# Performance work log

Hardware: AMD Instinct MI355X
Metric: run time of the kernel (lower is better)

## Reference

```python
import jax, jax.numpy as jnp
import numpy as np

B, S, E, H = 2, 2048, 1024, 16  # batch, max_seq_length, embedding_dim, num_heads
D = E // H  # head dim = 64


def setup_inputs() -> dict:
    key = jax.random.key(0)
    ks = jax.random.split(key, 7)
    scale = 0.02
    return {
        "inputs": jax.random.normal(ks[0], (B, S, E), jnp.float32),
        "embbeding_V": jax.random.normal(ks[1], (B, S, E), jnp.float32),
        "embbeding_K": jax.random.normal(ks[2], (B, S, E), jnp.float32),
        "Wq": jax.random.normal(ks[3], (E, E), jnp.float32) * scale,
        "Wk": jax.random.normal(ks[4], (E, E), jnp.float32) * scale,
        "Wv": jax.random.normal(ks[5], (E, E), jnp.float32) * scale,
        "Wo": jax.random.normal(ks[6], (E, E), jnp.float32) * scale,
    }


def reference(inputs, embbeding_V, embbeding_K, Wq, Wk, Wv, Wo):
    b = inputs.shape[0]
    # repeat last token of `inputs` to max_seq_length: [b, S, E]
    x = jnp.broadcast_to(inputs[:, -1, :][:, None, :], (b, S, E))
    # torch Linear(bias=False): y = x @ W.T ; split heads -> [b, H, S, D]
    q = (x @ Wq.T).reshape(b, S, H, D).transpose(0, 2, 1, 3)
    k = (embbeding_K @ Wk.T).reshape(b, S, H, D).transpose(0, 2, 1, 3)
    v = (embbeding_V @ Wv.T).reshape(b, S, H, D).transpose(0, 2, 1, 3)
    # UNSCALED attention (faithful to source: no 1/sqrt(d))
    s = jnp.einsum("bhqd,bhkd->bhqk", q, k)
    p = jax.nn.softmax(s, axis=-1)
    o = jnp.einsum("bhqk,bhkd->bhqd", p, v)
    # transpose(1,2) then reshape to [b, S, E]
    o = o.transpose(0, 2, 1, 3).reshape(b, S, E)
    return o @ Wo.T
```

## Files before the change

kernel.cpp:

```cpp
#include <hip/hip_runtime.h>
#include <hip/hip_bf16.h>

constexpr int B = 2, S = 2048, E = 1024, H = 16, D = 64;
constexpr int E4 = E / 4;

__global__ void k_qvec(const float4* __restrict__ x, const float4* __restrict__ Wq,
                       float* __restrict__ q_vec) {
  int blk = blockIdx.x;
  int b = blk >> 7, n0 = (blk & 127) * 8;
  int tid = threadIdx.x;
  int nl = tid >> 5, es = tid & 31;
  const float4* xr = x + ((size_t)b * S + (S - 1)) * E4;
  const float4* wr = Wq + (size_t)(n0 + nl) * E4;
  float acc = 0.f;
#pragma unroll
  for (int j = 0; j < 8; ++j) {
    float4 a = xr[es + 32 * j];
    float4 w = wr[es + 32 * j];
    acc += a.x * w.x + a.y * w.y + a.z * w.z + a.w * w.w;
  }
#pragma unroll
  for (int o = 16; o > 0; o >>= 1) acc += __shfl_xor(acc, o, 64);
  if (es == 0) q_vec[b * E + n0 + nl] = acc;
}

__global__ void k_wkq(const float* __restrict__ q_vec, const float* __restrict__ Wk,
                      float* __restrict__ wkq, float* __restrict__ rowsum) {
  int blk = blockIdx.x;
  int eo = blk & 7;
  int bh = blk >> 3;
  int h = bh & 15;
  int tid = threadIdx.x;
  __shared__ float qh[D];
  if (tid < D) qh[tid] = q_vec[(bh >> 4) * E + h * D + tid];
  if (eo == 0 && tid == 0) rowsum[bh] = 0.f;
  __syncthreads();
  int e = eo * 128 + tid;
  const float* wp = Wk + (size_t)h * D * E + e;
  float acc = 0.f;
#pragma unroll 8
  for (int d = 0; d < D; ++d) acc += qh[d] * wp[(size_t)d * E];
  wkq[(size_t)bh * E + e] = acc;
}

__global__ __launch_bounds__(128) void k_scores_exp(const float4* __restrict__ embK,
                                                    const float4* __restrict__ wkq4,
                                                    float* __restrict__ p,
                                                    float* __restrict__ rowsum) {
  __shared__ float4 wl[H * E4];
  __shared__ float hsum[16];
  int blk = blockIdx.x;
  int b = blk >> 7, k0 = (blk & 127) * 16;
  int tid = threadIdx.x;
#pragma unroll
  for (int j = 0; j < 32; ++j)
    wl[j * 128 + tid] = wkq4[(size_t)b * (H * E4) + j * 128 + tid];
  if (tid < 16) hsum[tid] = 0.f;
  __syncthreads();
  int kp = tid >> 4, es = tid & 15;
  int ka = k0 + kp, kb = k0 + 8 + kp;
  const float4* ea = embK + ((size_t)b * S + ka) * E4;
  const float4* eb = embK + ((size_t)b * S + kb) * E4;
  float4 va[16], vb[16];
#pragma unroll
  for (int j = 0; j < 16; ++j) { va[j] = ea[es + 16 * j]; vb[j] = eb[es + 16 * j]; }
#pragma unroll 1
  for (int h = 0; h < H; ++h) {
    float aa = 0.f, ab = 0.f;
#pragma unroll
    for (int j = 0; j < 16; ++j) {
      float4 w = wl[h * 256 + es + 16 * j];
      aa += va[j].x * w.x + va[j].y * w.y + va[j].z * w.z + va[j].w * w.w;
      ab += vb[j].x * w.x + vb[j].y * w.y + vb[j].z * w.z + vb[j].w * w.w;
    }
#pragma unroll
    for (int o = 8; o > 0; o >>= 1) {
      aa += __shfl_xor(aa, o, 64);
      ab += __shfl_xor(ab, o, 64);
    }
    if (es == 0) {
      float pa = __expf(aa), pb = __expf(ab);
      float* pr = p + ((size_t)(b * H + h)) * S;
      pr[ka] = pa;
      pr[kb] = pb;
      atomicAdd(&hsum[h], pa + pb);
    }
  }
  __syncthreads();
  if (tid < 16) atomicAdd(&rowsum[b * H + tid], hsum[tid]);
}

__global__ __launch_bounds__(256) void k_ctx_part(const float4* __restrict__ embV,
                                                  const float* __restrict__ p,
                                                  const float* __restrict__ rowsum,
                                                  float4* __restrict__ part) {
  int b = blockIdx.x, eo = blockIdx.y, kz = blockIdx.z;
  int tid = threadIdx.x;
  int e4l = tid & 31, ksub = tid >> 5;
  int k0 = kz * 128;
  __shared__ float pl[16 * 128];
  __shared__ float sinv[16];
  if (tid < 16) sinv[tid] = 1.f / rowsum[b * H + tid];
  __syncthreads();
  for (int i = tid; i < 16 * 128; i += 256) {
    int h = i >> 7, kk = i & 127;
    pl[i] = p[((size_t)(b * H + h)) * S + k0 + kk] * sinv[h];
  }
  __syncthreads();
  int e4 = eo * 32 + e4l;
  float4 acc[H];
#pragma unroll
  for (int h = 0; h < H; ++h) acc[h] = make_float4(0.f, 0.f, 0.f, 0.f);
  int kb = ksub * 16;
  for (int i = 0; i < 16; ++i) {
    int kk = kb + i;
    float4 v = embV[((size_t)b * S + k0 + kk) * E4 + e4];
#pragma unroll
    for (int h = 0; h < H; ++h) {
      float pv = pl[h * 128 + kk];
      acc[h].x += pv * v.x; acc[h].y += pv * v.y;
      acc[h].z += pv * v.z; acc[h].w += pv * v.w;
    }
  }
#pragma unroll
  for (int h = 0; h < H; ++h) {
    acc[h].x += __shfl_xor(acc[h].x, 32, 64);
    acc[h].y += __shfl_xor(acc[h].y, 32, 64);
    acc[h].z += __shfl_xor(acc[h].z, 32, 64);
    acc[h].w += __shfl_xor(acc[h].w, 32, 64);
  }
  if ((tid & 63) < 32) {
    int pz = kz * 4 + (tid >> 6);
#pragma unroll
    for (int h = 0; h < H; ++h)
      part[((size_t)(pz * B + b) * H + h) * E4 + e4] = acc[h];
  }
}

__global__ __launch_bounds__(128) void k_reduce(const float4* __restrict__ part,
                                                float4* __restrict__ ctx4) {
  int b = blockIdx.x, h = blockIdx.y, eo = blockIdx.z;
  int tid = threadIdx.x;
  int e4l = tid & 31, psub = tid >> 5;
  int e4 = eo * 32 + e4l;
  const size_t pstride = (size_t)B * H * E4;
  const float4* pp = part + ((size_t)b * H + h) * E4 + e4 + psub * 16 * pstride;
  float4 acc = make_float4(0.f, 0.f, 0.f, 0.f);
#pragma unroll
  for (int j = 0; j < 16; ++j) {
    float4 c = pp[j * pstride];
    acc.x += c.x; acc.y += c.y; acc.z += c.z; acc.w += c.w;
  }
  __shared__ float4 red[128];
  red[tid] = acc;
  __syncthreads();
  if (tid < 32) {
    float4 a0 = red[tid], a1 = red[tid + 32], a2 = red[tid + 64], a3 = red[tid + 96];
    float4 r = make_float4(a0.x + a1.x + a2.x + a3.x, a0.y + a1.y + a2.y + a3.y,
                           a0.z + a1.z + a2.z + a3.z, a0.w + a1.w + a2.w + a3.w);
    ctx4[((size_t)b * H + h) * E4 + e4] = r;
  }
}

__global__ void k_ovec_wave(const float* __restrict__ ctx, const float4* __restrict__ Wv4,
                            float* __restrict__ o_vec) {
  int gw = (blockIdx.x * blockDim.x + threadIdx.x) >> 6;
  int lane = threadIdx.x & 63;
  int b = gw >> 10, nn = gw & 1023;
  const float4* xr = (const float4*)(ctx + ((size_t)(b * H + (nn >> 6))) * E);
  const float4* wr = Wv4 + (size_t)nn * E4;
  float acc = 0.f;
#pragma unroll
  for (int j = 0; j < 4; ++j) {
    float4 a = xr[lane + 64 * j];
    float4 w = wr[lane + 64 * j];
    acc += a.x * w.x + a.y * w.y + a.z * w.z + a.w * w.w;
  }
#pragma unroll
  for (int o = 32; o > 0; o >>= 1) acc += __shfl_xor(acc, o, 64);
  if (lane == 0) o_vec[gw] = acc;
}

__global__ void k_outvec(const float* __restrict__ o_vec, const float4* __restrict__ Wo4,
                         float* __restrict__ out_vec) {
  int gw = (blockIdx.x * blockDim.x + threadIdx.x) >> 6;
  int lane = threadIdx.x & 63;
  int b = gw >> 10, nn = gw & 1023;
  const float4* xr = (const float4*)(o_vec + (size_t)b * E);
  const float4* wr = Wo4 + (size_t)nn * E4;
  float acc = 0.f;
#pragma unroll
  for (int j = 0; j < 4; ++j) {
    float4 a = xr[lane + 64 * j];
    float4 w = wr[lane + 64 * j];
    acc += a.x * w.x + a.y * w.y + a.z * w.z + a.w * w.w;
  }
#pragma unroll
  for (int o = 32; o > 0; o >>= 1) acc += __shfl_xor(acc, o, 64);
  if (lane == 0) out_vec[gw] = acc;
}

__global__ void k_bcast(const float4* __restrict__ ov4, float4* __restrict__ out4) {
  int base = blockIdx.x * 1024 + threadIdx.x;
#pragma unroll
  for (int r = 0; r < 4; ++r) {
    int g = base + r * 256;
    out4[g] = ov4[(g >> 19) * E4 + (g & 255)];
  }
}

extern "C" void kernel_launch(void* const* d_in, const int* in_sizes, int n_in,
                              void* d_out, int out_size, void* d_ws, size_t ws_size,
                              hipStream_t stream) {
  const float* inputs = (const float*)d_in[0];
  const float* embV   = (const float*)d_in[1];
  const float* embK   = (const float*)d_in[2];
  const float* Wq     = (const float*)d_in[3];
  const float* Wk     = (const float*)d_in[4];
  const float* Wv     = (const float*)d_in[5];
  const float* Wo     = (const float*)d_in[6];

  float* ws      = (float*)d_ws;
  float* q_vec   = ws;
  float* wkq     = q_vec + B * E;
  float* p       = wkq + B * H * E;
  float* rowsum  = p + B * H * S;
  float* o_vec   = rowsum + 64;
  float* out_vec = o_vec + B * E;
  float* part    = out_vec + B * E;
  float* ctx     = part + 64 * B * H * E;

  k_qvec<<<256, 256, 0, stream>>>((const float4*)inputs, (const float4*)Wq, q_vec);
  k_wkq<<<256, 128, 0, stream>>>(q_vec, Wk, wkq, rowsum);
  k_scores_exp<<<256, 128, 0, stream>>>((const float4*)embK, (const float4*)wkq,
                                        p, rowsum);
  k_ctx_part<<<dim3(B, 8, 16), 256, 0, stream>>>((const float4*)embV, p, rowsum,
                                                 (float4*)part);
  k_reduce<<<dim3(B, H, 8), 128, 0, stream>>>((const float4*)part, (float4*)ctx);
  k_ovec_wave<<<512, 256, 0, stream>>>(ctx, (const float4*)Wv, o_vec);
  k_outvec<<<512, 256, 0, stream>>>(o_vec, (const float4*)Wo, out_vec);
  k_bcast<<<1024, 256, 0, stream>>>((const float4*)out_vec, (float4*)d_out);
}
```

Before: 148.4 us.

## Retile context partial sums to halve partials and defer softmax normalization

The context-partial kernel now covers 256 keys per block with 16 e4 lanes per row and interleaved key assignment. This halves the number of partial slices written and then re-read by the reduce kernel. Softmax division by the row sum moves from the per-element P staging into the output-vector kernel, removing a sync and a per-element multiply. The tradeoff is narrower 256-byte row segments per load and an extra shuffle stage in the reduction.

```diff
diff --git a/kernel.cpp b/kernel.cpp
--- a/kernel.cpp
+++ b/kernel.cpp
@@ -92,45 +92,45 @@
 
 __global__ __launch_bounds__(256) void k_ctx_part(const float4* __restrict__ embV,
                                                   const float* __restrict__ p,
-                                                  const float* __restrict__ rowsum,
                                                   float4* __restrict__ part) {
   int b = blockIdx.x, eo = blockIdx.y, kz = blockIdx.z;
   int tid = threadIdx.x;
-  int e4l = tid & 31, ksub = tid >> 5;
-  int k0 = kz * 128;
-  __shared__ float pl[16 * 128];
-  __shared__ float sinv[16];
-  if (tid < 16) sinv[tid] = 1.f / rowsum[b * H + tid];
-  __syncthreads();
-  for (int i = tid; i < 16 * 128; i += 256) {
-    int h = i >> 7, kk = i & 127;
-    pl[i] = p[((size_t)(b * H + h)) * S + k0 + kk] * sinv[h];
-  }
-  __syncthreads();
-  int e4 = eo * 32 + e4l;
+  int e4l = tid & 15, ks = tid >> 4;
+  int k0 = kz * 256;
+  __shared__ float pl[16 * 256];
+  for (int i = tid; i < 16 * 256; i += 256) {
+    int h = i >> 8, kk = i & 255;
+    pl[i] = p[((size_t)(b * H + h)) * S + k0 + kk];
+  }
+  __syncthreads();
+  int e4 = eo * 16 + e4l;
   float4 acc[H];
 #pragma unroll
   for (int h = 0; h < H; ++h) acc[h] = make_float4(0.f, 0.f, 0.f, 0.f);
-  int kb = ksub * 16;
   for (int i = 0; i < 16; ++i) {
-    int kk = kb + i;
+    int kk = ks + 16 * i;
     float4 v = embV[((size_t)b * S + k0 + kk) * E4 + e4];
 #pragma unroll
     for (int h = 0; h < H; ++h) {
-      float pv = pl[h * 128 + kk];
+      float pv = pl[h * 256 + kk];
       acc[h].x += pv * v.x; acc[h].y += pv * v.y;
       acc[h].z += pv * v.z; acc[h].w += pv * v.w;
     }
   }
 #pragma unroll
   for (int h = 0; h < H; ++h) {
+    acc[h].x += __shfl_xor(acc[h].x, 16, 64);
+    acc[h].y += __shfl_xor(acc[h].y, 16, 64);
+    acc[h].z += __shfl_xor(acc[h].z, 16, 64);
+    acc[h].w += __shfl_xor(acc[h].w, 16, 64);
     acc[h].x += __shfl_xor(acc[h].x, 32, 64);
     acc[h].y += __shfl_xor(acc[h].y, 32, 64);
     acc[h].z += __shfl_xor(acc[h].z, 32, 64);
     acc[h].w += __shfl_xor(acc[h].w, 32, 64);
   }
-  if ((tid & 63) < 32) {
-    int pz = kz * 4 + (tid >> 6);
+  int lane = tid & 63, w = tid >> 6;
+  if (lane < 16) {
+    int pz = kz * 4 + w;
 #pragma unroll
     for (int h = 0; h < H; ++h)
       part[((size_t)(pz * B + b) * H + h) * E4 + e4] = acc[h];
@@ -144,10 +144,10 @@
   int e4l = tid & 31, psub = tid >> 5;
   int e4 = eo * 32 + e4l;
   const size_t pstride = (size_t)B * H * E4;
-  const float4* pp = part + ((size_t)b * H + h) * E4 + e4 + psub * 16 * pstride;
+  const float4* pp = part + ((size_t)b * H + h) * E4 + e4 + (size_t)psub * 8 * pstride;
   float4 acc = make_float4(0.f, 0.f, 0.f, 0.f);
 #pragma unroll
-  for (int j = 0; j < 16; ++j) {
+  for (int j = 0; j < 8; ++j) {
     float4 c = pp[j * pstride];
     acc.x += c.x; acc.y += c.y; acc.z += c.z; acc.w += c.w;
   }
@@ -163,11 +163,12 @@
 }
 
 __global__ void k_ovec_wave(const float* __restrict__ ctx, const float4* __restrict__ Wv4,
-                            float* __restrict__ o_vec) {
+                            const float* __restrict__ rowsum, float* __restrict__ o_vec) {
   int gw = (blockIdx.x * blockDim.x + threadIdx.x) >> 6;
   int lane = threadIdx.x & 63;
   int b = gw >> 10, nn = gw & 1023;
-  const float4* xr = (const float4*)(ctx + ((size_t)(b * H + (nn >> 6))) * E);
+  int bh = b * H + (nn >> 6);
+  const float4* xr = (const float4*)(ctx + (size_t)bh * E);
   const float4* wr = Wv4 + (size_t)nn * E4;
   float acc = 0.f;
 #pragma unroll
@@ -178,7 +179,7 @@
   }
 #pragma unroll
   for (int o = 32; o > 0; o >>= 1) acc += __shfl_xor(acc, o, 64);
-  if (lane == 0) o_vec[gw] = acc;
+  if (lane == 0) o_vec[gw] = acc / rowsum[bh];
 }
 
 __global__ void k_outvec(const float* __restrict__ o_vec, const float4* __restrict__ Wo4,
@@ -228,16 +229,15 @@
   float* o_vec   = rowsum + 64;
   float* out_vec = o_vec + B * E;
   float* part    = out_vec + B * E;
-  float* ctx     = part + 64 * B * H * E;
+  float* ctx     = part + 32 * B * H * E;
 
   k_qvec<<<256, 256, 0, stream>>>((const float4*)inputs, (const float4*)Wq, q_vec);
   k_wkq<<<256, 128, 0, stream>>>(q_vec, Wk, wkq, rowsum);
   k_scores_exp<<<256, 128, 0, stream>>>((const float4*)embK, (const float4*)wkq,
                                         p, rowsum);
-  k_ctx_part<<<dim3(B, 8, 16), 256, 0, stream>>>((const float4*)embV, p, rowsum,
-                                                 (float4*)part);
+  k_ctx_part<<<dim3(B, 16, 8), 256, 0, stream>>>((const float4*)embV, p, (float4*)part);
   k_reduce<<<dim3(B, H, 8), 128, 0, stream>>>((const float4*)part, (float4*)ctx);
-  k_ovec_wave<<<512, 256, 0, stream>>>(ctx, (const float4*)Wv, o_vec);
+  k_ovec_wave<<<512, 256, 0, stream>>>(ctx, (const float4*)Wv, rowsum, o_vec);
   k_outvec<<<512, 256, 0, stream>>>(o_vec, (const float4*)Wo, out_vec);
   k_bcast<<<1024, 256, 0, stream>>>((const float4*)out_vec, (float4*)d_out);
 }
```

Result: faster. 144.7 us (-2.5%).
